# Optimization experiments

Measured on AMD Instinct MI355X. Metric: run time of the kernel, lower is better.

The kernel has to match this reference:

```python
import jax, jax.numpy as jnp
import numpy as np

B, L, N = 16, 512, 32          # batch, seq_length, feature_size
E = 128                        # embed_size == frequency_size (number_frequency=1)
EMB = 8                        # embedding_dim
FCH = 64                       # fc_hidden_dim
H = 256                        # hidden_size
PRE = 96                       # pre_length
LAMBDA = 0.01                  # sparsity_threshold
SCALE = 0.02                   # init_scale


def softshrink(v, lambd=LAMBDA):
    return jnp.where(v > lambd, v - lambd, jnp.where(v < -lambd, v + lambd, 0.0))


def setup_inputs() -> dict:
    key = jax.random.key(0)
    ks = jax.random.split(key, 16)
    f32 = jnp.float32
    return {
        "x": jax.random.normal(ks[0], (B, L, N), f32),
        "emb": jax.random.normal(ks[1], (1, E), f32),
        "w0": SCALE * jax.random.normal(ks[2], (2, E, E), f32),
        "b0": SCALE * jax.random.normal(ks[3], (2, E), f32),
        "w1": SCALE * jax.random.normal(ks[4], (2, E, E), f32),
        "b1": SCALE * jax.random.normal(ks[5], (2, E), f32),
        "w2": SCALE * jax.random.normal(ks[6], (2, E, E), f32),
        "b2": SCALE * jax.random.normal(ks[7], (2, E), f32),
        "emb10": jax.random.normal(ks[8], (L, EMB), f32),
        "fc1_w": jax.random.normal(ks[9], (FCH, E * EMB), f32) / np.sqrt(E * EMB),
        "fc1_b": jnp.zeros((FCH,), f32),
        "fc2_w": jax.random.normal(ks[10], (H, FCH), f32) / np.sqrt(FCH),
        "fc2_b": jnp.zeros((H,), f32),
        "fc3_w": jax.random.normal(ks[11], (PRE, H), f32) / np.sqrt(H),
        "fc3_b": jnp.zeros((PRE,), f32),
    }


def _diag(w):
    # einsum 'bli,ii->bli' multiplies by the DIAGONAL of w only
    return jnp.diagonal(w, axis1=-2, axis2=-1)


def reference(x, emb, w0, b0, w1, b1, w2, b2, emb10,
              fc1_w, fc1_b, fc2_w, fc2_b, fc3_w, fc3_b):
    Bb = x.shape[0]
    xt = jnp.transpose(x, (0, 2, 1)).reshape(Bb, -1)          # [B, N*L]
    tok = xt[:, :, None] * emb                                 # [B, N*L, E]
    xf = jnp.fft.rfft(tok, axis=1, norm="ortho")               # [B, N*L//2+1, E] complex
    bias = xf

    # --- fourierGC (faithful to the torch op ordering, incl. o_real reuse) ---
    relu = jax.nn.relu
    d00, d01 = _diag(w0[0]), _diag(w0[1])
    o_r = relu(xf.real * d00 - xf.imag * d01 + b0[0])
    o_i = relu(xf.imag * d00 + xf.real * d01 + b0[1])
    prev = softshrink(jnp.stack([o_r, o_i], axis=-1))

    # middle layer (num_layers=3 -> one): note o_i uses the UPDATED o_r, as in torch
    d10, d11 = _diag(w1[0]), _diag(w1[1])
    o_r_new = relu(o_r * d10 - o_i * d11 + b1[0])
    o_i = relu(o_i * d10 + o_r_new * d11 + b1[1])
    o_r = o_r_new
    prev = softshrink(jnp.stack([o_r, o_i], axis=-1)) + prev

    # last layer
    d20, d21 = _diag(w2[0]), _diag(w2[1])
    o_r_new = relu(o_r * d20 - o_i * d21 + b2[0])
    o_i = relu(o_i * d20 + o_r_new * d21 + b2[1])
    z = softshrink(jnp.stack([o_r_new, o_i], axis=-1)) + prev
    zc = jax.lax.complex(z[..., 0], z[..., 1])

    xf = zc + bias
    xt = jnp.fft.irfft(xf, n=N * L, axis=1, norm="ortho")      # [B, N*L, E]
    xt = xt.reshape(Bb, N, L, E)
    xt = jnp.transpose(xt, (0, 1, 3, 2))                        # [B, N, E, L]
    h = jnp.matmul(xt, emb10)                                   # [B, N, E, EMB]
    h = h.reshape(Bb, N, E * EMB)

    lrelu = lambda v: jax.nn.leaky_relu(v, 0.01)
    h = lrelu(h @ fc1_w.T + fc1_b)
    h = lrelu(h @ fc2_w.T + fc2_b)
    out = h @ fc3_w.T + fc3_b                                   # [B, N, PRE]
    return out[:, 0, :]                                         # target_idx = 0
```

## Files before the change

kernel.cpp:

```cpp
#include <hip/hip_runtime.h>
#include <math.h>

#define Bsz   16
#define Lseq  512
#define Nfeat 32
#define E     128
#define EMB   8
#define FCH   64
#define Hd    256
#define PRE   96
#define M     16384
#define MH    8193
#define LAMBDA 0.01f

#define OFF_G   0
#define OFF_CS  524288
#define OFF_P   655376
#define OFF_H0  2752528

#define TWO_PI_M   3.83495196971410293e-4f
#define TWO_PI_128 4.90873852123405245e-2f

__global__ __launch_bounds__(256)
void k_prep(const float* __restrict__ x, const float* __restrict__ emb10,
            float* __restrict__ ws) {
  __shared__ float smem[Lseq * EMB];
  int bid = blockIdx.x, tid = threadIdx.x;
  if (bid < 257) {
    for (int i = tid; i < Lseq * EMB; i += 256) smem[i] = emb10[i];
    __syncthreads();
    int floc = tid >> 5, tl = tid & 31;
    #pragma unroll
    for (int ff = 0; ff < 4; ++ff) {
      int f = bid * 32 + ff * 8 + floc;
      if (f <= 8192) {
        float ca[EMB], sa[EMB];
        #pragma unroll
        for (int m = 0; m < EMB; ++m) { ca[m] = 0.f; sa[m] = 0.f; }
        #pragma unroll 4
        for (int i = 0; i < 16; ++i) {
          int t = tl + 32 * i;
          int k = (f * t) & (M - 1);
          float ss, cc;
          sincosf((float)k * TWO_PI_M, &ss, &cc);
          const float* er = smem + t * EMB;
          #pragma unroll
          for (int m = 0; m < EMB; ++m) {
            ca[m] = fmaf(cc, er[m], ca[m]);
            sa[m] = fmaf(ss, er[m], sa[m]);
          }
        }
        #pragma unroll
        for (int off = 16; off >= 1; off >>= 1) {
          #pragma unroll
          for (int m = 0; m < EMB; ++m) {
            ca[m] += __shfl_xor(ca[m], off, 64);
            sa[m] += __shfl_xor(sa[m], off, 64);
          }
        }
        if (tl == 0) {
          float wf = (f == 0 || f == 8192) ? (1.0f / 128.0f) : (2.0f / 128.0f);
          float* o = ws + OFF_CS + f * 16;
          #pragma unroll
          for (int m = 0; m < EMB; ++m) { o[m] = ca[m] * wf; o[8 + m] = sa[m] * wf; }
        }
      }
    }
  } else {
    int v = bid - 257;
    int b = v >> 6, t1base = (v & 63) << 1;
    int t1loc = tid >> 7, idx = tid & 127;
    {
      int t = (t1base + t1loc) + 128 * idx;
      int n = t >> 9, l = t & 511;
      smem[t1loc * 128 + idx] = x[b * (Lseq * Nfeat) + l * Nfeat + n];
    }
    __syncthreads();
    int f1 = idx, t1 = t1base + t1loc;
    float s1, c1; sincosf((float)f1 * TWO_PI_128, &s1, &c1);
    float c2 = c1 * c1 - s1 * s1, s2 = 2.f * s1 * c1;
    float cA = 1.f, sA = 0.f, cB = c1, sB = s1;
    float grA = 0.f, giA = 0.f, grB = 0.f, giB = 0.f;
    const float* xc = smem + t1loc * 128;
    #pragma unroll 8
    for (int t2 = 0; t2 < 128; t2 += 2) {
      float x0 = xc[t2], x1 = xc[t2 + 1];
      grA = fmaf(x0, cA, grA); giA = fmaf(x0, -sA, giA);
      grB = fmaf(x1, cB, grB); giB = fmaf(x1, -sB, giB);
      float cn = cA * c2 - sA * s2; sA = sA * c2 + cA * s2; cA = cn;
      cn = cB * c2 - sB * s2;       sB = sB * c2 + cB * s2; cB = cn;
    }
    float gr = grA + grB, gi = giA + giB;
    float sb, cb; sincosf((float)(f1 * t1) * TWO_PI_M, &sb, &cb);
    float grr = gr * cb + gi * sb;
    float gii = gi * cb - gr * sb;
    float* G = ws + OFF_G + ((b * 128 + f1) * 128 + t1) * 2;
    G[0] = grr;
    G[1] = gii;
  }
}

__global__ __launch_bounds__(256)
void k_gcf(const float* __restrict__ emb,
           const float* __restrict__ w0, const float* __restrict__ b0,
           const float* __restrict__ w1, const float* __restrict__ b1,
           const float* __restrict__ w2, const float* __restrict__ b2,
           float* __restrict__ ws) {
  int f1 = blockIdx.x, b = blockIdx.y, tid = threadIdx.x;
  int nf2 = (f1 == 0) ? 65 : 64;
  __shared__ float2 Gs[128];
  __shared__ float Xp[4][65][2];
  __shared__ float CSs[65 * 16];
  {
    const float2* gsrc = (const float2*)(ws + OFF_G + (b * 128 + f1) * 256);
    if (tid < 128) Gs[tid] = gsrc[tid];
    for (int j = tid; j < nf2 * 16; j += 256) {
      int i = j >> 4, m = j & 15;
      CSs[j] = ws[OFF_CS + (f1 + 128 * i) * 16 + m];
    }
  }
  __syncthreads();
  {
    int f2 = tid & 63, q = tid >> 6;
    int r = (f2 * q) & 3;
    float c = (r == 0) ? 1.f : (r == 2) ? -1.f : 0.f;
    float s = (r == 1) ? 1.f : (r == 3) ? -1.f : 0.f;
    float s1, c1; sincosf((float)f2 * TWO_PI_128, &s1, &c1);
    float xr = 0.f, xi = 0.f;
    int t1 = q * 32;
    #pragma unroll 8
    for (int k = 0; k < 32; ++k) {
      float2 g = Gs[t1 + k];
      xr = fmaf(g.x, c, xr); xr = fmaf(g.y, s, xr);
      xi = fmaf(g.y, c, xi); xi = fmaf(-g.x, s, xi);
      float cn = c * c1 - s * s1; s = s * c1 + c * s1; c = cn;
    }
    Xp[q][f2][0] = xr; Xp[q][f2][1] = xi;
    if (f1 == 0 && f2 == 0) {
      float er = 0.f, ei = 0.f;
      #pragma unroll 8
      for (int k = 0; k < 32; ++k) {
        float2 g = Gs[t1 + k];
        float sg = ((t1 + k) & 1) ? -1.f : 1.f;
        er = fmaf(g.x, sg, er); ei = fmaf(g.y, sg, ei);
      }
      Xp[q][64][0] = er; Xp[q][64][1] = ei;
    }
  }
  __syncthreads();
  int e = tid & 127, fh = tid >> 7;
  float se  = emb[e] * (1.0f / 128.0f);
  float d00 = w0[e * 129], d01 = w0[E * E + e * 129];
  float c00 = b0[e],       c01 = b0[E + e];
  float d10 = w1[e * 129], d11 = w1[E * E + e * 129];
  float c10 = b1[e],       c11 = b1[E + e];
  float d20 = w2[e * 129], d21 = w2[E * E + e * 129];
  float c20 = b2[e],       c21 = b2[E + e];
  float acc[EMB];
  #pragma unroll
  for (int m = 0; m < EMB; ++m) acc[m] = 0.f;

  for (int i = fh; i < nf2; i += 2) {
    float xr = ((Xp[0][i][0] + Xp[1][i][0]) + (Xp[2][i][0] + Xp[3][i][0])) * se;
    float xi = ((Xp[0][i][1] + Xp[1][i][1]) + (Xp[2][i][1] + Xp[3][i][1])) * se;
    float or0 = fmaxf(fmaf(xr, d00, fmaf(-xi, d01, c00)), 0.f);
    float oi0 = fmaxf(fmaf(xi, d00, fmaf(xr, d01, c01)), 0.f);
    float pr = fmaxf(or0 - LAMBDA, 0.f), pi = fmaxf(oi0 - LAMBDA, 0.f);
    float or1 = fmaxf(fmaf(or0, d10, fmaf(-oi0, d11, c10)), 0.f);
    float oi1 = fmaxf(fmaf(oi0, d10, fmaf(or1, d11, c11)), 0.f);
    pr += fmaxf(or1 - LAMBDA, 0.f); pi += fmaxf(oi1 - LAMBDA, 0.f);
    float or2 = fmaxf(fmaf(or1, d20, fmaf(-oi1, d21, c20)), 0.f);
    float oi2 = fmaxf(fmaf(oi1, d20, fmaf(or2, d21, c21)), 0.f);
    float zr = fmaxf(or2 - LAMBDA, 0.f) + pr;
    float zi = fmaxf(oi2 - LAMBDA, 0.f) + pi;
    const float* cs = &CSs[i * 16];
    #pragma unroll
    for (int m = 0; m < EMB; ++m)
      acc[m] = fmaf(zr, cs[m], fmaf(-zi, cs[8 + m], acc[m]));
  }
  __syncthreads();
  float* red = CSs;
  if (fh == 1) {
    #pragma unroll
    for (int m = 0; m < EMB; ++m) red[e * EMB + m] = acc[m];
  }
  __syncthreads();
  if (fh == 0) {
    float* P = ws + OFF_P + (f1 * 16 + b) * (E * EMB) + e * EMB;
    #pragma unroll
    for (int m = 0; m < EMB; ++m) P[m] = acc[m] + red[e * EMB + m];
  }
}

__global__ __launch_bounds__(256)
void k_red(float* __restrict__ ws) {
  int bid = blockIdx.x;
  int b = bid >> 4, kq = bid & 15;
  int tid = threadIdx.x;
  int kk = tid & 63, f1g = tid >> 6;
  int k = kq * 64 + kk;
  const float* P = ws + OFF_P + b * (E * EMB) + k;
  float a = 0.f;
  #pragma unroll 8
  for (int j = 0; j < 32; ++j)
    a += P[(f1g * 32 + j) * (16 * E * EMB)];
  __shared__ float sh[256];
  sh[tid] = a;
  __syncthreads();
  if (tid < 64)
    ws[OFF_H0 + b * (E * EMB) + k] = sh[tid] + sh[tid + 64] + sh[tid + 128] + sh[tid + 192];
}

__global__ __launch_bounds__(1024)
void k_fc(const float* __restrict__ x, const float* __restrict__ emb,
          const float* __restrict__ emb10,
          const float* __restrict__ fc1w, const float* __restrict__ fc1b,
          const float* __restrict__ fc2w, const float* __restrict__ fc2b,
          const float* __restrict__ fc3w, const float* __restrict__ fc3b,
          const float* __restrict__ ws, float* __restrict__ out) {
  int b = blockIdx.x;
  __shared__ float h0s[E * EMB];
  __shared__ float h1s[FCH];
  __shared__ float h2s[Hd];
  __shared__ float hxs[EMB];
  __shared__ float scratch[1024];
  int tid = threadIdx.x;
  int lane = tid & 63, w = tid >> 6;
  {
    int m = tid & 7, g = tid >> 3;
    float p = 0.f;
    #pragma unroll
    for (int l = g; l < Lseq; l += 128)
      p = fmaf(x[b * (Lseq * Nfeat) + l * Nfeat], emb10[l * EMB + m], p);
    scratch[tid] = p;
  }
  __syncthreads();
  if (tid < 8) {
    float s = 0.f;
    #pragma unroll 16
    for (int g = 0; g < 128; ++g) s += scratch[g * 8 + tid];
    hxs[tid] = s;
  }
  __syncthreads();
  h0s[tid] = ws[OFF_H0 + b * (E * EMB) + tid] + emb[tid >> 3] * hxs[tid & 7];
  __syncthreads();
  #pragma unroll
  for (int oo = 0; oo < 4; ++oo) {
    int o = oo * 16 + w;
    const float* wr = fc1w + o * (E * EMB);
    float a = 0.f;
    #pragma unroll
    for (int j = 0; j < 16; ++j) a = fmaf(h0s[lane + 64 * j], wr[lane + 64 * j], a);
    #pragma unroll
    for (int off = 32; off >= 1; off >>= 1) a += __shfl_xor(a, off, 64);
    if (lane == 0) { float v = a + fc1b[o]; h1s[o] = v > 0.f ? v : 0.01f * v; }
  }
  __syncthreads();
  #pragma unroll
  for (int oo = 0; oo < 16; ++oo) {
    int o = oo * 16 + w;
    float a = h1s[lane] * fc2w[o * FCH + lane];
    #pragma unroll
    for (int off = 32; off >= 1; off >>= 1) a += __shfl_xor(a, off, 64);
    if (lane == 0) { float v = a + fc2b[o]; h2s[o] = v > 0.f ? v : 0.01f * v; }
  }
  __syncthreads();
  #pragma unroll
  for (int oo = 0; oo < 6; ++oo) {
    int o = oo * 16 + w;
    const float* wr = fc3w + o * Hd;
    float a = 0.f;
    #pragma unroll
    for (int j = 0; j < 4; ++j) a = fmaf(h2s[lane + 64 * j], wr[lane + 64 * j], a);
    #pragma unroll
    for (int off = 32; off >= 1; off >>= 1) a += __shfl_xor(a, off, 64);
    if (lane == 0) out[b * PRE + o] = a + fc3b[o];
  }
}

extern "C" void kernel_launch(void* const* d_in, const int* in_sizes, int n_in,
                              void* d_out, int out_size, void* d_ws, size_t ws_size,
                              hipStream_t stream) {
  const float* x     = (const float*)d_in[0];
  const float* emb   = (const float*)d_in[1];
  const float* w0    = (const float*)d_in[2];
  const float* b0    = (const float*)d_in[3];
  const float* w1    = (const float*)d_in[4];
  const float* b1    = (const float*)d_in[5];
  const float* w2    = (const float*)d_in[6];
  const float* b2    = (const float*)d_in[7];
  const float* emb10 = (const float*)d_in[8];
  const float* fc1w  = (const float*)d_in[9];
  const float* fc1b  = (const float*)d_in[10];
  const float* fc2w  = (const float*)d_in[11];
  const float* fc2b  = (const float*)d_in[12];
  const float* fc3w  = (const float*)d_in[13];
  const float* fc3b  = (const float*)d_in[14];
  float* ws  = (float*)d_ws;
  float* out = (float*)d_out;

  k_prep<<<dim3(1281), 256, 0, stream>>>(x, emb10, ws);
  k_gcf<<<dim3(128, Bsz), 256, 0, stream>>>(emb, w0, b0, w1, b1, w2, b2, ws);
  k_red<<<dim3(256), 256, 0, stream>>>(ws);
  k_fc<<<dim3(Bsz), 1024, 0, stream>>>(x, emb, emb10, fc1w, fc1b, fc2w, fc2b,
                                       fc3w, fc3b, ws, out);
}
```

Baseline: 160.5 us.

## Fold partial-sum reduction into FC kernel and streamline gcf smem usage

Removes the separate k_red launch: k_fc now sums the 128 per-f1 partials directly from the workspace. In k_gcf the per-quarter DFT partials are combined with wave shuffles instead of a shared array, the G tile is padded to avoid bank conflicts, and the CS coefficients are read straight from global memory with uniform (scalar) addresses instead of being staged in LDS. The last-layer relu/softshrink is simplified algebraically. Each k_fc thread now issues a 128-long strided global read chain, which could lengthen that single 16-block kernel.

```diff
diff --git a/kernel.cpp b/kernel.cpp
--- a/kernel.cpp
+++ b/kernel.cpp
@@ -16,7 +16,6 @@
 #define OFF_G   0
 #define OFF_CS  524288
 #define OFF_P   655376
-#define OFF_H0  2752528
 
 #define TWO_PI_M   3.83495196971410293e-4f
 #define TWO_PI_128 4.90873852123405245e-2f
@@ -108,43 +107,48 @@
            float* __restrict__ ws) {
   int f1 = blockIdx.x, b = blockIdx.y, tid = threadIdx.x;
   int nf2 = (f1 == 0) ? 65 : 64;
-  __shared__ float2 Gs[128];
-  __shared__ float Xp[4][65][2];
-  __shared__ float CSs[65 * 16];
+  __shared__ float2 Gs[132];
+  __shared__ float2 Xs[65];
+  __shared__ float red[E * EMB];
+  if (tid < 128)
+    Gs[(tid >> 5) * 33 + (tid & 31)] =
+        ((const float2*)(ws + OFF_G + (b * 128 + f1) * 256))[tid];
+  __syncthreads();
   {
-    const float2* gsrc = (const float2*)(ws + OFF_G + (b * 128 + f1) * 256);
-    if (tid < 128) Gs[tid] = gsrc[tid];
-    for (int j = tid; j < nf2 * 16; j += 256) {
-      int i = j >> 4, m = j & 15;
-      CSs[j] = ws[OFF_CS + (f1 + 128 * i) * 16 + m];
-    }
-  }
-  __syncthreads();
-  {
-    int f2 = tid & 63, q = tid >> 6;
+    int lane = tid & 63, w = tid >> 6;
+    int q = lane >> 4, f2l = lane & 15;
+    int f2 = w * 16 + f2l;
     int r = (f2 * q) & 3;
     float c = (r == 0) ? 1.f : (r == 2) ? -1.f : 0.f;
     float s = (r == 1) ? 1.f : (r == 3) ? -1.f : 0.f;
     float s1, c1; sincosf((float)f2 * TWO_PI_128, &s1, &c1);
     float xr = 0.f, xi = 0.f;
-    int t1 = q * 32;
+    const float2* g = Gs + q * 33;
     #pragma unroll 8
     for (int k = 0; k < 32; ++k) {
-      float2 g = Gs[t1 + k];
-      xr = fmaf(g.x, c, xr); xr = fmaf(g.y, s, xr);
-      xi = fmaf(g.y, c, xi); xi = fmaf(-g.x, s, xi);
+      float2 gv = g[k];
+      xr = fmaf(gv.x, c, xr); xr = fmaf(gv.y, s, xr);
+      xi = fmaf(gv.y, c, xi); xi = fmaf(-gv.x, s, xi);
       float cn = c * c1 - s * s1; s = s * c1 + c * s1; c = cn;
     }
-    Xp[q][f2][0] = xr; Xp[q][f2][1] = xi;
-    if (f1 == 0 && f2 == 0) {
+    xr += __shfl_xor(xr, 16, 64); xi += __shfl_xor(xi, 16, 64);
+    xr += __shfl_xor(xr, 32, 64); xi += __shfl_xor(xi, 32, 64);
+    if (lane < 16) Xs[f2] = make_float2(xr, xi);
+    if (f1 == 0 && tid < 32) {
       float er = 0.f, ei = 0.f;
-      #pragma unroll 8
-      for (int k = 0; k < 32; ++k) {
-        float2 g = Gs[t1 + k];
-        float sg = ((t1 + k) & 1) ? -1.f : 1.f;
-        er = fmaf(g.x, sg, er); ei = fmaf(g.y, sg, ei);
+      #pragma unroll
+      for (int j = 0; j < 4; ++j) {
+        int t1v = tid * 4 + j;
+        float2 gv = Gs[(t1v >> 5) * 33 + (t1v & 31)];
+        float sg = (j & 1) ? -1.f : 1.f;
+        er = fmaf(gv.x, sg, er); ei = fmaf(gv.y, sg, ei);
       }
-      Xp[q][64][0] = er; Xp[q][64][1] = ei;
+      #pragma unroll
+      for (int off = 1; off <= 16; off <<= 1) {
+        er += __shfl_xor(er, off, 64);
+        ei += __shfl_xor(ei, off, 64);
+      }
+      if (tid == 0) Xs[64] = make_float2(er, ei);
     }
   }
   __syncthreads();
@@ -159,27 +163,29 @@
   float acc[EMB];
   #pragma unroll
   for (int m = 0; m < EMB; ++m) acc[m] = 0.f;
+  const float* csbase = ws + OFF_CS + f1 * 16;
 
   for (int i = fh; i < nf2; i += 2) {
-    float xr = ((Xp[0][i][0] + Xp[1][i][0]) + (Xp[2][i][0] + Xp[3][i][0])) * se;
-    float xi = ((Xp[0][i][1] + Xp[1][i][1]) + (Xp[2][i][1] + Xp[3][i][1])) * se;
+    int iu = __builtin_amdgcn_readfirstlane(i);
+    const float* cs = csbase + (iu << 11);
+    float2 X = Xs[i];
+    float xr = X.x * se, xi = X.y * se;
     float or0 = fmaxf(fmaf(xr, d00, fmaf(-xi, d01, c00)), 0.f);
     float oi0 = fmaxf(fmaf(xi, d00, fmaf(xr, d01, c01)), 0.f);
     float pr = fmaxf(or0 - LAMBDA, 0.f), pi = fmaxf(oi0 - LAMBDA, 0.f);
     float or1 = fmaxf(fmaf(or0, d10, fmaf(-oi0, d11, c10)), 0.f);
     float oi1 = fmaxf(fmaf(oi0, d10, fmaf(or1, d11, c11)), 0.f);
     pr += fmaxf(or1 - LAMBDA, 0.f); pi += fmaxf(oi1 - LAMBDA, 0.f);
-    float or2 = fmaxf(fmaf(or1, d20, fmaf(-oi1, d21, c20)), 0.f);
-    float oi2 = fmaxf(fmaf(oi1, d20, fmaf(or2, d21, c21)), 0.f);
-    float zr = fmaxf(or2 - LAMBDA, 0.f) + pr;
-    float zi = fmaxf(oi2 - LAMBDA, 0.f) + pi;
-    const float* cs = &CSs[i * 16];
+    float u2r = fmaf(or1, d20, fmaf(-oi1, d21, c20));
+    float or2 = fmaxf(u2r, 0.f);
+    float u2i = fmaf(oi1, d20, fmaf(or2, d21, c21));
+    float zr = fmaxf(u2r - LAMBDA, 0.f) + pr;
+    float zi = fmaxf(u2i - LAMBDA, 0.f) + pi;
     #pragma unroll
     for (int m = 0; m < EMB; ++m)
       acc[m] = fmaf(zr, cs[m], fmaf(-zi, cs[8 + m], acc[m]));
   }
   __syncthreads();
-  float* red = CSs;
   if (fh == 1) {
     #pragma unroll
     for (int m = 0; m < EMB; ++m) red[e * EMB + m] = acc[m];
@@ -190,25 +196,6 @@
     #pragma unroll
     for (int m = 0; m < EMB; ++m) P[m] = acc[m] + red[e * EMB + m];
   }
-}
-
-__global__ __launch_bounds__(256)
-void k_red(float* __restrict__ ws) {
-  int bid = blockIdx.x;
-  int b = bid >> 4, kq = bid & 15;
-  int tid = threadIdx.x;
-  int kk = tid & 63, f1g = tid >> 6;
-  int k = kq * 64 + kk;
-  const float* P = ws + OFF_P + b * (E * EMB) + k;
-  float a = 0.f;
-  #pragma unroll 8
-  for (int j = 0; j < 32; ++j)
-    a += P[(f1g * 32 + j) * (16 * E * EMB)];
-  __shared__ float sh[256];
-  sh[tid] = a;
-  __syncthreads();
-  if (tid < 64)
-    ws[OFF_H0 + b * (E * EMB) + k] = sh[tid] + sh[tid + 64] + sh[tid + 128] + sh[tid + 192];
 }
 
 __global__ __launch_bounds__(1024)
@@ -223,58 +210,65 @@
   __shared__ float h1s[FCH];
   __shared__ float h2s[Hd];
   __shared__ float hxs[EMB];
-  __shared__ float scratch[1024];
   int tid = threadIdx.x;
   int lane = tid & 63, w = tid >> 6;
   {
-    int m = tid & 7, g = tid >> 3;
+    int m = lane & 7, g8 = lane >> 3;
+    int gg = w * 8 + g8;
     float p = 0.f;
     #pragma unroll
-    for (int l = g; l < Lseq; l += 128)
+    for (int l = gg; l < Lseq; l += 128)
       p = fmaf(x[b * (Lseq * Nfeat) + l * Nfeat], emb10[l * EMB + m], p);
-    scratch[tid] = p;
-  }
+    p += __shfl_xor(p, 8, 64);
+    p += __shfl_xor(p, 16, 64);
+    p += __shfl_xor(p, 32, 64);
+    if (lane < 8) h2s[w * 8 + lane] = p;
+  }
+  const float* P = ws + OFF_P + b * (E * EMB) + tid;
+  float a = 0.f;
+  #pragma unroll 16
+  for (int j = 0; j < 128; ++j) a += P[j * (16 * E * EMB)];
   __syncthreads();
   if (tid < 8) {
     float s = 0.f;
-    #pragma unroll 16
-    for (int g = 0; g < 128; ++g) s += scratch[g * 8 + tid];
+    #pragma unroll
+    for (int wv = 0; wv < 16; ++wv) s += h2s[wv * 8 + tid];
     hxs[tid] = s;
   }
   __syncthreads();
-  h0s[tid] = ws[OFF_H0 + b * (E * EMB) + tid] + emb[tid >> 3] * hxs[tid & 7];
+  h0s[tid] = a + emb[tid >> 3] * hxs[tid & 7];
   __syncthreads();
   #pragma unroll
   for (int oo = 0; oo < 4; ++oo) {
     int o = oo * 16 + w;
     const float* wr = fc1w + o * (E * EMB);
-    float a = 0.f;
-    #pragma unroll
-    for (int j = 0; j < 16; ++j) a = fmaf(h0s[lane + 64 * j], wr[lane + 64 * j], a);
-    #pragma unroll
-    for (int off = 32; off >= 1; off >>= 1) a += __shfl_xor(a, off, 64);
-    if (lane == 0) { float v = a + fc1b[o]; h1s[o] = v > 0.f ? v : 0.01f * v; }
+    float acc = 0.f;
+    #pragma unroll
+    for (int j = 0; j < 16; ++j) acc = fmaf(h0s[lane + 64 * j], wr[lane + 64 * j], acc);
+    #pragma unroll
+    for (int off = 32; off >= 1; off >>= 1) acc += __shfl_xor(acc, off, 64);
+    if (lane == 0) { float v = acc + fc1b[o]; h1s[o] = v > 0.f ? v : 0.01f * v; }
   }
   __syncthreads();
   #pragma unroll
   for (int oo = 0; oo < 16; ++oo) {
     int o = oo * 16 + w;
-    float a = h1s[lane] * fc2w[o * FCH + lane];
-    #pragma unroll
-    for (int off = 32; off >= 1; off >>= 1) a += __shfl_xor(a, off, 64);
-    if (lane == 0) { float v = a + fc2b[o]; h2s[o] = v > 0.f ? v : 0.01f * v; }
+    float acc = h1s[lane] * fc2w[o * FCH + lane];
+    #pragma unroll
+    for (int off = 32; off >= 1; off >>= 1) acc += __shfl_xor(acc, off, 64);
+    if (lane == 0) { float v = acc + fc2b[o]; h2s[o] = v > 0.f ? v : 0.01f * v; }
   }
   __syncthreads();
   #pragma unroll
   for (int oo = 0; oo < 6; ++oo) {
     int o = oo * 16 + w;
     const float* wr = fc3w + o * Hd;
-    float a = 0.f;
-    #pragma unroll
-    for (int j = 0; j < 4; ++j) a = fmaf(h2s[lane + 64 * j], wr[lane + 64 * j], a);
-    #pragma unroll
-    for (int off = 32; off >= 1; off >>= 1) a += __shfl_xor(a, off, 64);
-    if (lane == 0) out[b * PRE + o] = a + fc3b[o];
+    float acc = 0.f;
+    #pragma unroll
+    for (int j = 0; j < 4; ++j) acc = fmaf(h2s[lane + 64 * j], wr[lane + 64 * j], acc);
+    #pragma unroll
+    for (int off = 32; off >= 1; off >>= 1) acc += __shfl_xor(acc, off, 64);
+    if (lane == 0) out[b * PRE + o] = acc + fc3b[o];
   }
 }
 
@@ -301,7 +295,6 @@
 
   k_prep<<<dim3(1281), 256, 0, stream>>>(x, emb10, ws);
   k_gcf<<<dim3(128, Bsz), 256, 0, stream>>>(emb, w0, b0, w1, b1, w2, b2, ws);
-  k_red<<<dim3(256), 256, 0, stream>>>(ws);
   k_fc<<<dim3(Bsz), 1024, 0, stream>>>(x, emb, emb10, fc1w, fc1b, fc2w, fc2b,
                                        fc3w, fc3b, ws, out);
 }
```

Result: faster. 153.4 us (-4.4%).
